# Kernel optimization log

Hardware: AMD Instinct MI355X
Metric: run time of the kernel (lower is better)

## Reference

```python
import jax, jax.numpy as jnp
import numpy as np

B, D, L, K = 16, 64, 8192, 512


def setup_inputs() -> dict:
    key = jax.random.key(0)
    k1, k2 = jax.random.split(key)
    feature_vectors = jax.random.normal(k1, (B, D, L), dtype=jnp.float32)
    embeddings = jax.random.normal(k2, (D, K), dtype=jnp.float32)  # codebook: latent_dim x num_embeddings
    return {"feature_vectors": feature_vectors, "embeddings": embeddings}


def reference(feature_vectors, embeddings):
    # feature_vectors: (B, D, L); embeddings: (D, K)
    b, d, l = feature_vectors.shape
    k = embeddings.shape[1]
    # tokens: (B*L, D)
    x = jnp.transpose(feature_vectors, (0, 2, 1)).reshape(-1, d)
    x_sq = jnp.sum(x * x, axis=1, keepdims=True)              # (N, 1)
    e_sq = jnp.sum(embeddings * embeddings, axis=0)[None, :]  # (1, K)
    sqdist = x_sq - 2.0 * (x @ embeddings) + e_sq             # (N, K)
    idx_flat = jnp.argmin(sqdist, axis=-1)                    # (N,)
    # gather nearest codebook vectors
    emb_out = jnp.take(embeddings.T, idx_flat, axis=0)        # (N, D)
    closest_embeddings = jnp.transpose(emb_out.reshape(b, l, d), (0, 2, 1))  # (B, D, L)
    closest_indices = idx_flat.reshape(b, l)                  # (B, L)
    return closest_embeddings, closest_indices
```

## Files before the change

### kernel.cpp

```cpp
#include <hip/hip_runtime.h>
#include <float.h>

#define B_ 16
#define D_ 64
#define L_ 8192
#define K_ 512
#define NBLOCKS 256
#define TILE_TOK 128
#define TILES_PER_BLOCK 4
#define EPS 0.0625f


typedef __attribute__((ext_vector_type(8))) _Float16 half8;
typedef __attribute__((ext_vector_type(4))) float    f32x4;

__device__ __forceinline__ unsigned f32_sortable(float x) {
    unsigned u = __float_as_uint(x);
    return u ^ (((int)u >> 31) | 0x80000000u);
}

__global__ __launch_bounds__(512, 1)
void vq_mfma_kernel(const float* __restrict__ X, const float* __restrict__ E,
                    float* __restrict__ out_emb, float* __restrict__ out_idx)
{
    __shared__ __align__(16) short eF[32768];
    __shared__ __align__(16) short xAh[8192];
    __shared__ float xT[64][132];
    __shared__ float esq_s[K_];
    __shared__ int   bestk_s[TILE_TOK];

    const int tid  = threadIdx.x;
    const int lane = tid & 63;
    const int wave = tid >> 6;
    const int lo4  = lane & 15;
    const int hi4  = lane >> 4;

    {
        float s = 0.f;
        #pragma unroll
        for (int c = 0; c < 4; ++c) {
            float v[16];
            #pragma unroll
            for (int m = 0; m < 16; ++m) v[m] = E[(c * 16 + m) * K_ + tid];
            #pragma unroll
            for (int m = 0; m < 16; ++m) {
                float sq = v[m] * v[m];
                asm volatile("" : "+v"(sq));
                s = s + sq;
            }
        }
        esq_s[tid] = s;
    }

    {
        int fl = tid & 63, pr = tid >> 6;
        #pragma unroll
        for (int it = 0; it < 8; ++it) {
            int idx = it * 8 + pr;
            int blk = idx >> 1, kh = idx & 1;
            half8 h;
            #pragma unroll
            for (int j = 0; j < 8; ++j)
                h[j] = (_Float16)E[(kh * 32 + (fl >> 4) * 8 + j) * K_ + blk * 16 + (fl & 15)];
            ((half8*)eF)[(blk * 2 + kh) * 64 + fl] = h;
        }
    }

    for (int t = 0; t < TILES_PER_BLOCK; ++t) {
        int tile = blockIdx.x * TILES_PER_BLOCK + t;
        int b  = tile >> 6;
        int l0 = (tile & 63) << 7;

        __syncthreads();

        {
            const float* xb = X + ((size_t)(b * 64 + wave * 8)) * L_ + l0 + lane;
            #pragma unroll
            for (int hh = 0; hh < 2; ++hh) {
                int tok = hh * 64 + lane;
                float xv[8];
                #pragma unroll
                for (int r = 0; r < 8; ++r) xv[r] = xb[(size_t)r * L_ + hh * 64];
                #pragma unroll
                for (int r = 0; r < 8; ++r) xT[wave * 8 + r][tok] = xv[r];
                half8 h8;
                #pragma unroll
                for (int r = 0; r < 8; ++r) h8[r] = (_Float16)xv[r];
                int tb = tok >> 4, kh = wave >> 2;
                int fl = (wave & 3) * 16 + (tok & 15);
                ((half8*)xAh)[(tb * 2 + kh) * 64 + fl] = h8;
            }
        }
        __syncthreads();

        float xs;
        {
            int token = wave * 16 + lo4;
            int ja = 2 * hi4, jb = ja + 1;
            float ra = 0.f, rb = 0.f;
            #pragma unroll
            for (int m = 0; m < 8; ++m) {
                float va = xT[m * 8 + ja][token];
                float vb = xT[m * 8 + jb][token];
                float sa = va * va, sb = vb * vb;
                asm volatile("" : "+v"(sa));
                asm volatile("" : "+v"(sb));
                ra = ra + sa;
                rb = rb + sb;
            }
            float s = ra + rb;
            s = s + __shfl_xor(s, 16, 64);
            s = s + __shfl_xor(s, 32, 64);
            xs = __shfl(s, lo4, 64);
        }

        half8 bh0 = ((const half8*)xAh)[(wave * 2 + 0) * 64 + lane];
        half8 bh1 = ((const half8*)xAh)[(wave * 2 + 1) * 64 + lane];

        float m1 = FLT_MAX, m2 = FLT_MAX;
        int   k1 = 0x7FFFFFFF;
        #pragma unroll 8
        for (int blk = 0; blk < 32; ++blk) {
            half8 ah0 = ((const half8*)eF)[(blk * 2 + 0) * 64 + lane];
            half8 ah1 = ((const half8*)eF)[(blk * 2 + 1) * 64 + lane];
            f32x4 c = {0.f, 0.f, 0.f, 0.f};
            c = __builtin_amdgcn_mfma_f32_16x16x32_f16(ah0, bh0, c, 0, 0, 0);
            c = __builtin_amdgcn_mfma_f32_16x16x32_f16(ah1, bh1, c, 0, 0, 0);
            float4 es4 = *reinterpret_cast<const float4*>(&esq_s[blk * 16 + hi4 * 4]);
            float es[4] = {es4.x, es4.y, es4.z, es4.w};
            #pragma unroll
            for (int r = 0; r < 4; ++r) {
                float sc = (xs - 2.0f * c[r]) + es[r];
                int   cd = blk * 16 + hi4 * 4 + r;
                if (sc < m1)      { m2 = m1; m1 = sc; k1 = cd; }
                else              { m2 = fminf(m2, sc); }
            }
        }

        #pragma unroll
        for (int off = 16; off < 64; off <<= 1) {
            float ov = __shfl_xor(m1, off, 64);
            int   ok = __shfl_xor(k1, off, 64);
            float o2 = __shfl_xor(m2, off, 64);
            float n2 = fminf(fminf(m2, o2), fmaxf(m1, ov));
            if (ov < m1 || (ov == m1 && ok < k1)) { m1 = ov; k1 = ok; }
            m2 = n2;
        }

        bool mine = (lane < 16);
        bool flg  = mine && (m2 <= m1 + EPS);
        if (mine && !flg) bestk_s[wave * 16 + lane] = k1;
        unsigned long long bal = __ballot(flg);

        while (bal) {
            int tk_local = (int)__builtin_ctzll(bal);
            bal &= bal - 1;
            int token = wave * 16 + tk_local;
            float xs_e = __shfl(xs, tk_local, 64);
            float d0 = 0.f, d1 = 0.f, d2 = 0.f, d3 = 0.f;
            float d4 = 0.f, d5 = 0.f, d6 = 0.f, d7 = 0.f;
            const float* Ep = E + 8 * lane;
            #pragma unroll 4
            for (int d = 0; d < 64; ++d) {
                float xv = xT[d][token];
                float4 e0 = *reinterpret_cast<const float4*>(Ep + d * K_);
                float4 e1 = *reinterpret_cast<const float4*>(Ep + d * K_ + 4);
                d0 = fmaf(xv, e0.x, d0); d1 = fmaf(xv, e0.y, d1);
                d2 = fmaf(xv, e0.z, d2); d3 = fmaf(xv, e0.w, d3);
                d4 = fmaf(xv, e1.x, d4); d5 = fmaf(xv, e1.y, d5);
                d6 = fmaf(xv, e1.z, d6); d7 = fmaf(xv, e1.w, d7);
            }
            float4 qa = *reinterpret_cast<const float4*>(&esq_s[8 * lane]);
            float4 qb = *reinterpret_cast<const float4*>(&esq_s[8 * lane + 4]);
            float sc[8];
            sc[0] = (xs_e - 2.0f * d0) + qa.x; sc[1] = (xs_e - 2.0f * d1) + qa.y;
            sc[2] = (xs_e - 2.0f * d2) + qa.z; sc[3] = (xs_e - 2.0f * d3) + qa.w;
            sc[4] = (xs_e - 2.0f * d4) + qb.x; sc[5] = (xs_e - 2.0f * d5) + qb.y;
            sc[6] = (xs_e - 2.0f * d6) + qb.z; sc[7] = (xs_e - 2.0f * d7) + qb.w;
            unsigned long long pk = ~0ULL;
            #pragma unroll
            for (int j = 0; j < 8; ++j) {
                unsigned long long p =
                    ((unsigned long long)f32_sortable(sc[j]) << 32) |
                    (unsigned)(8 * lane + j);
                if (p < pk) pk = p;
            }
            #pragma unroll
            for (int off = 1; off < 64; off <<= 1) {
                unsigned long long o = __shfl_xor(pk, off, 64);
                if (o < pk) pk = o;
            }
            if (lane == 0)
                bestk_s[token] = (int)(unsigned)(pk & 0xFFFFFFFFULL);
        }
        __syncthreads();

        {
            int d  = tid >> 3;
            int q8 = tid & 7;
            #pragma unroll
            for (int it = 0; it < 4; ++it) {
                int quad = q8 + it * 8;
                int i4 = quad * 4;
                int k0 = bestk_s[i4],     kk1 = bestk_s[i4 + 1];
                int k2 = bestk_s[i4 + 2], k3  = bestk_s[i4 + 3];
                float4 v;
                v.x = E[d * K_ + k0];  v.y = E[d * K_ + kk1];
                v.z = E[d * K_ + k2];  v.w = E[d * K_ + k3];
                *reinterpret_cast<float4*>(out_emb + ((size_t)(b * 64 + d)) * L_ + l0 + i4) = v;
            }
        }
        if (tid < TILE_TOK)
            out_idx[(size_t)b * L_ + l0 + tid] = (float)bestk_s[tid];
    }
}

extern "C" void kernel_launch(void* const* d_in, const int* in_sizes, int n_in,
                              void* d_out, int out_size, void* d_ws, size_t ws_size,
                              hipStream_t stream) {
    const float* X = (const float*)d_in[0];
    const float* E = (const float*)d_in[1];
    float* out     = (float*)d_out;
    float* out_emb = out;
    float* out_idx = out + (size_t)B_ * D_ * L_;
    vq_mfma_kernel<<<NBLOCKS, 512, 0, stream>>>(X, E, out_emb, out_idx);
}
```

Baseline: 66.31 us.

## Drop token LDS staging, load MFMA operands directly, raise occupancy to two blocks

Removes the xT/xAh/bestk shared buffers and their barriers. Each wave now loads its token fragments straight from global memory into MFMA registers, and the scoring drops the per-token ||x||^2 term because it does not change the argmin. The exact-recheck path rebuilds ||x||^2 and the x values from global memory, and the gather writes are done per lane from the k1 register. Less LDS use allows two blocks per CU with twice as many blocks, but the token loads are now strided global accesses and the output stores are scalar rather than float4.

```diff
diff --git a/kernel.cpp b/kernel.cpp
--- a/kernel.cpp
+++ b/kernel.cpp
@@ -5,9 +5,8 @@
 #define D_ 64
 #define L_ 8192
 #define K_ 512
-#define NBLOCKS 256
-#define TILE_TOK 128
-#define TILES_PER_BLOCK 4
+#define NBLOCKS 512
+#define TILES_PER_BLOCK 2
 #define EPS 0.0625f
 
 
@@ -19,15 +18,12 @@
     return u ^ (((int)u >> 31) | 0x80000000u);
 }
 
-__global__ __launch_bounds__(512, 1)
+__global__ __launch_bounds__(512, 2)
 void vq_mfma_kernel(const float* __restrict__ X, const float* __restrict__ E,
                     float* __restrict__ out_emb, float* __restrict__ out_idx)
 {
     __shared__ __align__(16) short eF[32768];
-    __shared__ __align__(16) short xAh[8192];
-    __shared__ float xT[64][132];
     __shared__ float esq_s[K_];
-    __shared__ int   bestk_s[TILE_TOK];
 
     const int tid  = threadIdx.x;
     const int lane = tid & 63;
@@ -36,86 +32,38 @@
     const int hi4  = lane >> 4;
 
     {
+        _Float16* eH = (_Float16*)eF;
         float s = 0.f;
-        #pragma unroll
-        for (int c = 0; c < 4; ++c) {
-            float v[16];
-            #pragma unroll
-            for (int m = 0; m < 16; ++m) v[m] = E[(c * 16 + m) * K_ + tid];
-            #pragma unroll
-            for (int m = 0; m < 16; ++m) {
-                float sq = v[m] * v[m];
-                asm volatile("" : "+v"(sq));
-                s = s + sq;
-            }
+        int code = tid;
+        int blk = code >> 4, c15 = code & 15;
+        #pragma unroll 8
+        for (int d = 0; d < D_; ++d) {
+            float v = E[d * K_ + code];
+            float sq = v * v;
+            asm volatile("" : "+v"(sq));
+            s = s + sq;
+            int kh = d >> 5, fl = ((d >> 3) & 3) * 16 + c15, j = d & 7;
+            eH[((blk * 2 + kh) * 64 + fl) * 8 + j] = (_Float16)v;
         }
-        esq_s[tid] = s;
+        esq_s[code] = s;
     }
-
-    {
-        int fl = tid & 63, pr = tid >> 6;
-        #pragma unroll
-        for (int it = 0; it < 8; ++it) {
-            int idx = it * 8 + pr;
-            int blk = idx >> 1, kh = idx & 1;
-            half8 h;
-            #pragma unroll
-            for (int j = 0; j < 8; ++j)
-                h[j] = (_Float16)E[(kh * 32 + (fl >> 4) * 8 + j) * K_ + blk * 16 + (fl & 15)];
-            ((half8*)eF)[(blk * 2 + kh) * 64 + fl] = h;
-        }
-    }
+    __syncthreads();
 
     for (int t = 0; t < TILES_PER_BLOCK; ++t) {
         int tile = blockIdx.x * TILES_PER_BLOCK + t;
         int b  = tile >> 6;
         int l0 = (tile & 63) << 7;
+        const int token = wave * 16 + lo4;
 
-        __syncthreads();
-
+        half8 bh0, bh1;
         {
-            const float* xb = X + ((size_t)(b * 64 + wave * 8)) * L_ + l0 + lane;
+            const float* xb = X + ((size_t)(b * 64 + hi4 * 8)) * L_ + l0 + token;
             #pragma unroll
-            for (int hh = 0; hh < 2; ++hh) {
-                int tok = hh * 64 + lane;
-                float xv[8];
-                #pragma unroll
-                for (int r = 0; r < 8; ++r) xv[r] = xb[(size_t)r * L_ + hh * 64];
-                #pragma unroll
-                for (int r = 0; r < 8; ++r) xT[wave * 8 + r][tok] = xv[r];
-                half8 h8;
-                #pragma unroll
-                for (int r = 0; r < 8; ++r) h8[r] = (_Float16)xv[r];
-                int tb = tok >> 4, kh = wave >> 2;
-                int fl = (wave & 3) * 16 + (tok & 15);
-                ((half8*)xAh)[(tb * 2 + kh) * 64 + fl] = h8;
+            for (int j = 0; j < 8; ++j) {
+                bh0[j] = (_Float16)xb[(size_t)j * L_];
+                bh1[j] = (_Float16)xb[(size_t)(32 + j) * L_];
             }
         }
-        __syncthreads();
-
-        float xs;
-        {
-            int token = wave * 16 + lo4;
-            int ja = 2 * hi4, jb = ja + 1;
-            float ra = 0.f, rb = 0.f;
-            #pragma unroll
-            for (int m = 0; m < 8; ++m) {
-                float va = xT[m * 8 + ja][token];
-                float vb = xT[m * 8 + jb][token];
-                float sa = va * va, sb = vb * vb;
-                asm volatile("" : "+v"(sa));
-                asm volatile("" : "+v"(sb));
-                ra = ra + sa;
-                rb = rb + sb;
-            }
-            float s = ra + rb;
-            s = s + __shfl_xor(s, 16, 64);
-            s = s + __shfl_xor(s, 32, 64);
-            xs = __shfl(s, lo4, 64);
-        }
-
-        half8 bh0 = ((const half8*)xAh)[(wave * 2 + 0) * 64 + lane];
-        half8 bh1 = ((const half8*)xAh)[(wave * 2 + 1) * 64 + lane];
 
         float m1 = FLT_MAX, m2 = FLT_MAX;
         int   k1 = 0x7FFFFFFF;
@@ -130,7 +78,7 @@
             float es[4] = {es4.x, es4.y, es4.z, es4.w};
             #pragma unroll
             for (int r = 0; r < 4; ++r) {
-                float sc = (xs - 2.0f * c[r]) + es[r];
+                float sc = fmaf(-2.0f, c[r], es[r]);
                 int   cd = blk * 16 + hi4 * 4 + r;
                 if (sc < m1)      { m2 = m1; m1 = sc; k1 = cd; }
                 else              { m2 = fminf(m2, sc); }
@@ -147,22 +95,32 @@
             m2 = n2;
         }
 
-        bool mine = (lane < 16);
-        bool flg  = mine && (m2 <= m1 + EPS);
-        if (mine && !flg) bestk_s[wave * 16 + lane] = k1;
-        unsigned long long bal = __ballot(flg);
-
+        unsigned long long bal = __ballot((lane < 16) && (m2 <= m1 + EPS));
         while (bal) {
-            int tk_local = (int)__builtin_ctzll(bal);
+            int tk = (int)__builtin_ctzll(bal);
             bal &= bal - 1;
-            int token = wave * 16 + tk_local;
-            float xs_e = __shfl(xs, tk_local, 64);
+            float xs_e;
+            {
+                int j = lane & 7;
+                float r = 0.f;
+                #pragma unroll
+                for (int m = 0; m < 8; ++m) {
+                    float v = X[((size_t)(b * 64 + m * 8 + j)) * L_ + l0 + wave * 16 + tk];
+                    float sq = v * v;
+                    asm volatile("" : "+v"(sq));
+                    r = r + sq;
+                }
+                r = r + __shfl_xor(r, 1, 64);
+                r = r + __shfl_xor(r, 2, 64);
+                r = r + __shfl_xor(r, 4, 64);
+                xs_e = r;
+            }
             float d0 = 0.f, d1 = 0.f, d2 = 0.f, d3 = 0.f;
             float d4 = 0.f, d5 = 0.f, d6 = 0.f, d7 = 0.f;
             const float* Ep = E + 8 * lane;
             #pragma unroll 4
             for (int d = 0; d < 64; ++d) {
-                float xv = xT[d][token];
+                float xv = X[((size_t)(b * 64 + d)) * L_ + l0 + wave * 16 + tk];
                 float4 e0 = *reinterpret_cast<const float4*>(Ep + d * K_);
                 float4 e1 = *reinterpret_cast<const float4*>(Ep + d * K_ + 4);
                 d0 = fmaf(xv, e0.x, d0); d1 = fmaf(xv, e0.y, d1);
@@ -190,28 +148,20 @@
                 unsigned long long o = __shfl_xor(pk, off, 64);
                 if (o < pk) pk = o;
             }
-            if (lane == 0)
-                bestk_s[token] = (int)(unsigned)(pk & 0xFFFFFFFFULL);
+            int k_ex = (int)(unsigned)(pk & 0xFFFFFFFFULL);
+            if (lo4 == tk) k1 = k_ex;
         }
-        __syncthreads();
 
         {
-            int d  = tid >> 3;
-            int q8 = tid & 7;
-            #pragma unroll
-            for (int it = 0; it < 4; ++it) {
-                int quad = q8 + it * 8;
-                int i4 = quad * 4;
-                int k0 = bestk_s[i4],     kk1 = bestk_s[i4 + 1];
-                int k2 = bestk_s[i4 + 2], k3  = bestk_s[i4 + 3];
-                float4 v;
-                v.x = E[d * K_ + k0];  v.y = E[d * K_ + kk1];
-                v.z = E[d * K_ + k2];  v.w = E[d * K_ + k3];
-                *reinterpret_cast<float4*>(out_emb + ((size_t)(b * 64 + d)) * L_ + l0 + i4) = v;
+            size_t obase = (size_t)b * 64 * L_ + l0 + token;
+            #pragma unroll 4
+            for (int dd = 0; dd < 16; ++dd) {
+                int d = hi4 * 16 + dd;
+                out_emb[obase + (size_t)d * L_] = E[d * K_ + k1];
             }
+            if (hi4 == 0)
+                out_idx[(size_t)b * L_ + l0 + token] = (float)k1;
         }
-        if (tid < TILE_TOK)
-            out_idx[(size_t)b * L_ + l0 + tid] = (float)bestk_s[tid];
     }
 }
 
```

Measured after the change: 71.69 us. 8.1% more time.
